# Performance work log

Hardware: AMD Instinct MI355X
Metric: run time of the kernel (lower is better)

Reference implementation:

```python
import math
import jax, jax.numpy as jnp
import numpy as np

IN_DIM, OUT_DIM = 256, 128
IN_SEQ, OUT_SEQ = 512, 512
NUM_BASIS = 16
LN_EPS = 1e-5
TWO_PI = 2.0 * math.pi


def _make_periods():
    # periods[i, j, g] = i*(out_dim*num_basis) + j*num_basis + g + 2
    i = np.arange(OUT_DIM)[:, None, None]
    j = np.arange(OUT_DIM)[None, :, None]
    g = np.arange(NUM_BASIS)[None, None, :]
    return jnp.asarray((i * (OUT_DIM * NUM_BASIS) + j * NUM_BASIS + g + 2).astype(np.float32))


def setup_inputs() -> dict:
    key = jax.random.key(0)
    kx, kM, kP, kL = jax.random.split(key, 4)
    x = jax.random.normal(kx, (IN_SEQ, IN_DIM), dtype=jnp.float32)
    M = jax.random.normal(kM, (OUT_DIM, IN_DIM), dtype=jnp.float32) * 0.5
    P = jax.random.normal(kP, (OUT_DIM, OUT_DIM, NUM_BASIS), dtype=jnp.float32) * 0.1
    Linker = jax.random.normal(kL, (IN_SEQ, OUT_SEQ), dtype=jnp.float32) * 0.1
    gamma = jnp.ones((OUT_DIM,), dtype=jnp.float32)
    beta = jnp.zeros((OUT_DIM,), dtype=jnp.float32)
    periods = _make_periods()  # (O, O, B) constant buffer
    return {"x": x, "M": M, "P": P, "Linker": Linker,
            "gamma": gamma, "beta": beta, "periods": periods}


def reference(x, M, P, Linker, gamma, beta, periods):
    # Projection: Z = x @ M.T  -> (S, O)
    Z = x @ M.T
    # LayerNorm over last dim
    mu = jnp.mean(Z, axis=-1, keepdims=True)
    var = jnp.mean(jnp.square(Z - mu), axis=-1, keepdims=True)
    Zn = (Z - mu) * jax.lax.rsqrt(var + LN_EPS) * gamma + beta
    # Position transform: T[k,i] = sum_{j,g} Zn[k,j] * P[i,j,g] * cos(2*pi*k / periods[i,j,g])
    k = jnp.arange(Z.shape[0], dtype=jnp.float32)[:, None, None, None]  # (S,1,1,1)
    phi = jnp.cos(TWO_PI * k / periods)  # (S, O, O, B)
    T = jnp.einsum('kj,ijg,kijg->ki', Zn, P, phi)  # (S, O)
    # Sequence transform: U = Linker.T @ T -> (out_seq, O)
    U = Linker.T @ T
    # 'shared' residual uses pre-LayerNorm projection x @ M.T
    residual = Linker.T @ Z
    return U + residual
```

## Files before the change

kernel.cpp:

```cpp
#include <hip/hip_runtime.h>

#define IN_DIM   256
#define OUT_DIM  128
#define IN_SEQ   512
#define OUT_SEQ  512
#define NUM_BASIS 16
#define LN_EPS   1e-5f

__global__ __launch_bounds__(256) void kA(const float* __restrict__ x,
                                          const float* __restrict__ M,
                                          const float* __restrict__ gamma,
                                          const float* __restrict__ beta,
                                          float* __restrict__ Zn,
                                          float* __restrict__ ZT) {
  const int k = blockIdx.x;
  const int t = threadIdx.x;
  __shared__ __align__(16) float xk[IN_DIM];
  __shared__ float red[256];
  __shared__ float stats[8];

  xk[t] = x[k * IN_DIM + t];
  __syncthreads();

  const int j = t & 127;
  const int h = t >> 7;
  const float4* __restrict__ M4 = reinterpret_cast<const float4*>(M + j * IN_DIM + h * 128);
  const float4* __restrict__ x4 = reinterpret_cast<const float4*>(xk + h * 128);
  float acc = 0.f;
#pragma unroll 8
  for (int c = 0; c < 32; ++c) {
    float4 m = M4[c];
    float4 xv = x4[c];
    acc = fmaf(m.x, xv.x, acc);
    acc = fmaf(m.y, xv.y, acc);
    acc = fmaf(m.z, xv.z, acc);
    acc = fmaf(m.w, xv.w, acc);
  }
  red[t] = acc;
  __syncthreads();

  float z = 0.f;
  if (t < 128) z = red[t] + red[t + 128];

  float s1 = (t < 128) ? z : 0.f;
  float s2 = (t < 128) ? z * z : 0.f;
#pragma unroll
  for (int m = 1; m < 64; m <<= 1) {
    s1 += __shfl_xor(s1, m);
    s2 += __shfl_xor(s2, m);
  }
  const int w = t >> 6;
  if ((t & 63) == 0) {
    stats[w] = s1;
    stats[4 + w] = s2;
  }
  __syncthreads();
  const float mu  = (stats[0] + stats[1] + stats[2] + stats[3]) * (1.f / 128.f);
  const float msq = (stats[4] + stats[5] + stats[6] + stats[7]) * (1.f / 128.f);
  const float rs  = rsqrtf(msq - mu * mu + LN_EPS);

  if (t < 128) {
    float zn = (z - mu) * rs * gamma[t] + beta[t];
    Zn[k * OUT_DIM + t] = zn;
    ZT[t * IN_SEQ + k] = z;
  }
}

__global__ __launch_bounds__(256) void kB(const float* __restrict__ P,
                                          const float* __restrict__ Zn,
                                          const float* __restrict__ ZT,
                                          float* __restrict__ V) {
  const int i  = blockIdx.y;
  const int k0 = blockIdx.x * 64;
  const int t  = threadIdx.x;

  __shared__ float2 pairs[OUT_DIM * NUM_BASIS];
  __shared__ float zn_lds[64 * 129];
  __shared__ float red[64 * 5];

  const float* __restrict__ Pi = P + i * (OUT_DIM * NUM_BASIS);
  const int pbase = i * (OUT_DIM * NUM_BASIS) + 2;
#pragma unroll
  for (int e = t; e < OUT_DIM * NUM_BASIS; e += 256) {
    float pw = Pi[e];
    float pinv = 1.0f / (float)(pbase + e);
    pairs[e] = make_float2(pw, pinv);
  }
#pragma unroll
  for (int m = 0; m < 32; ++m) {
    int idx = m * 256 + t;
    int r = idx >> 7;
    int j = idx & 127;
    zn_lds[r * 129 + j] = Zn[(k0 + r) * OUT_DIM + j];
  }
  __syncthreads();

  const int kl = t & 63;
  const int jq = t >> 6;
  const float kf = (float)(k0 + kl);
  const float* __restrict__ znrow = zn_lds + kl * 129;

  float acc = 0.f;
  for (int j = jq * 32; j < jq * 32 + 32; ++j) {
    float z = znrow[j];
    const float2* __restrict__ pp = pairs + j * NUM_BASIS;
    float accj = 0.f;
#pragma unroll
    for (int g = 0; g < NUM_BASIS; ++g) {
      float2 wv = pp[g];
      float ang = kf * wv.y;
      float fr  = __builtin_amdgcn_fractf(ang);
      float c   = __builtin_amdgcn_cosf(fr);
      accj = fmaf(wv.x, c, accj);
    }
    acc = fmaf(z, accj, acc);
  }

  red[kl * 5 + jq] = acc;
  __syncthreads();
  if (t < 64) {
    float s = red[t * 5 + 0] + red[t * 5 + 1] + red[t * 5 + 2] + red[t * 5 + 3];
    const int k = k0 + t;
    V[k * OUT_DIM + i] = s + ZT[i * IN_SEQ + k];
  }
}

__global__ __launch_bounds__(512) void kC(const float* __restrict__ L,
                                          const float* __restrict__ V,
                                          float* __restrict__ out) {
  const int s = blockIdx.x;
  const int t = threadIdx.x;
  const int i = t & 127;
  const int q = t >> 7;
  __shared__ float Lcol[IN_SEQ];
  __shared__ float red[4 * OUT_DIM];

  Lcol[t] = L[t * OUT_SEQ + s];
  __syncthreads();

  const int k0 = q * 128;
  float acc = 0.f;
#pragma unroll 8
  for (int kk = 0; kk < 128; ++kk) {
    const int k = k0 + kk;
    acc = fmaf(Lcol[k], V[k * OUT_DIM + i], acc);
  }
  red[q * OUT_DIM + i] = acc;
  __syncthreads();

  if (t < OUT_DIM) {
    out[s * OUT_DIM + t] =
        red[t] + red[OUT_DIM + t] + red[2 * OUT_DIM + t] + red[3 * OUT_DIM + t];
  }
}

extern "C" void kernel_launch(void* const* d_in, const int* in_sizes, int n_in,
                              void* d_out, int out_size, void* d_ws, size_t ws_size,
                              hipStream_t stream) {
  const float* x      = (const float*)d_in[0];
  const float* M      = (const float*)d_in[1];
  const float* P      = (const float*)d_in[2];
  const float* Linker = (const float*)d_in[3];
  const float* gamma  = (const float*)d_in[4];
  const float* beta   = (const float*)d_in[5];
  float* out = (float*)d_out;

  float* ws = (float*)d_ws;
  float* Zn = ws;
  float* ZT = ws + IN_SEQ * OUT_DIM;
  float* V  = ws + 2 * IN_SEQ * OUT_DIM;

  kA<<<dim3(IN_SEQ), dim3(256), 0, stream>>>(x, M, gamma, beta, Zn, ZT);
  kB<<<dim3(8, OUT_DIM), dim3(256), 0, stream>>>(P, Zn, ZT, V);
  kC<<<dim3(OUT_SEQ), dim3(512), 0, stream>>>(Linker, V, out);
}
```

Baseline: 43.96 us.

## Replace per-element cosine evaluation with a Chebyshev recurrence over sequence positions

The position-transform kernel is restructured so each thread owns one (i,j) pair and walks 64 consecutive k values. It uses the recurrence cos((k+1)θ) = 2cosθ·cos(kθ) − cos((k−1)θ) instead of a fract plus transcendental cos for every (k,j,g). Per-k partial sums are reduced across the j lanes with wave shuffles, and the shared-memory staging of P and Zn is removed. The aim is to drop the quarter-rate cosine cost. In exchange, the recurrence accumulates rounding error across steps, a reduction runs for every k, and the prefetch reads a few rows past the chunk end, including past the end of Zn for the last block.

```diff
diff --git a/kernel.cpp b/kernel.cpp
--- a/kernel.cpp
+++ b/kernel.cpp
@@ -6,6 +6,11 @@
 #define OUT_SEQ  512
 #define NUM_BASIS 16
 #define LN_EPS   1e-5f
+#define KC       64
+
+__device__ __forceinline__ float cosrev(float x) {
+  return __builtin_amdgcn_cosf(__builtin_amdgcn_fractf(x));
+}
 
 __global__ __launch_bounds__(256) void kA(const float* __restrict__ x,
                                           const float* __restrict__ M,
@@ -66,62 +71,76 @@
   }
 }
 
-__global__ __launch_bounds__(256) void kB(const float* __restrict__ P,
+__global__ __launch_bounds__(128) void kB(const float* __restrict__ P,
                                           const float* __restrict__ Zn,
                                           const float* __restrict__ ZT,
                                           float* __restrict__ V) {
   const int i  = blockIdx.y;
-  const int k0 = blockIdx.x * 64;
-  const int t  = threadIdx.x;
+  const int k0 = blockIdx.x * KC;
+  const int j  = threadIdx.x;
+  const int w  = j >> 6;
 
-  __shared__ float2 pairs[OUT_DIM * NUM_BASIS];
-  __shared__ float zn_lds[64 * 129];
-  __shared__ float red[64 * 5];
+  __shared__ float red[KC * 2];
 
-  const float* __restrict__ Pi = P + i * (OUT_DIM * NUM_BASIS);
-  const int pbase = i * (OUT_DIM * NUM_BASIS) + 2;
+  float Pv[NUM_BASIS], tc[NUM_BASIS], c0[NUM_BASIS], c1[NUM_BASIS];
+  {
+    const float4* __restrict__ P4 =
+        reinterpret_cast<const float4*>(P + (size_t)(i * OUT_DIM + j) * NUM_BASIS);
+    float4 pl[4] = {P4[0], P4[1], P4[2], P4[3]};
 #pragma unroll
-  for (int e = t; e < OUT_DIM * NUM_BASIS; e += 256) {
-    float pw = Pi[e];
-    float pinv = 1.0f / (float)(pbase + e);
-    pairs[e] = make_float2(pw, pinv);
+    for (int q = 0; q < 4; ++q) {
+      Pv[4 * q + 0] = pl[q].x;
+      Pv[4 * q + 1] = pl[q].y;
+      Pv[4 * q + 2] = pl[q].z;
+      Pv[4 * q + 3] = pl[q].w;
+    }
   }
+  const int pb = i * (OUT_DIM * NUM_BASIS) + j * NUM_BASIS + 2;
+  const float km1 = (float)(k0 - 1);
+  const float kcu = (float)k0;
 #pragma unroll
-  for (int m = 0; m < 32; ++m) {
-    int idx = m * 256 + t;
-    int r = idx >> 7;
-    int j = idx & 127;
-    zn_lds[r * 129 + j] = Zn[(k0 + r) * OUT_DIM + j];
-  }
-  __syncthreads();
-
-  const int kl = t & 63;
-  const int jq = t >> 6;
-  const float kf = (float)(k0 + kl);
-  const float* __restrict__ znrow = zn_lds + kl * 129;
-
-  float acc = 0.f;
-  for (int j = jq * 32; j < jq * 32 + 32; ++j) {
-    float z = znrow[j];
-    const float2* __restrict__ pp = pairs + j * NUM_BASIS;
-    float accj = 0.f;
-#pragma unroll
-    for (int g = 0; g < NUM_BASIS; ++g) {
-      float2 wv = pp[g];
-      float ang = kf * wv.y;
-      float fr  = __builtin_amdgcn_fractf(ang);
-      float c   = __builtin_amdgcn_cosf(fr);
-      accj = fmaf(wv.x, c, accj);
-    }
-    acc = fmaf(z, accj, acc);
+  for (int g = 0; g < NUM_BASIS; ++g) {
+    float pinv = 1.0f / (float)(pb + g);
+    tc[g] = 2.0f * __builtin_amdgcn_cosf(pinv);
+    c0[g] = cosrev(km1 * pinv);
+    c1[g] = cosrev(kcu * pinv);
   }
 
-  red[kl * 5 + jq] = acc;
+  const float* __restrict__ znj = Zn + j;
+  float buf[4];
+#pragma unroll
+  for (int r = 0; r < 4; ++r) buf[r] = znj[(k0 + r) * OUT_DIM];
+
+  for (int kg = 0; kg < KC / 4; ++kg) {
+    float nbuf[4];
+#pragma unroll
+    for (int r = 0; r < 4; ++r) {
+      nbuf[r] = znj[(k0 + (kg + 1) * 4 + r) * OUT_DIM];
+    }
+#pragma unroll
+    for (int r = 0; r < 4; ++r) {
+      float s = 0.f;
+#pragma unroll
+      for (int g = 0; g < NUM_BASIS; ++g) s = fmaf(Pv[g], c1[g], s);
+      float v = buf[r] * s;
+#pragma unroll
+      for (int m = 1; m < 64; m <<= 1) v += __shfl_xor(v, m);
+      if ((j & 63) == 0) red[(kg * 4 + r) * 2 + w] = v;
+#pragma unroll
+      for (int g = 0; g < NUM_BASIS; ++g) {
+        float cn = fmaf(tc[g], c1[g], -c0[g]);
+        c0[g] = c1[g];
+        c1[g] = cn;
+      }
+    }
+#pragma unroll
+    for (int r = 0; r < 4; ++r) buf[r] = nbuf[r];
+  }
+
   __syncthreads();
-  if (t < 64) {
-    float s = red[t * 5 + 0] + red[t * 5 + 1] + red[t * 5 + 2] + red[t * 5 + 3];
-    const int k = k0 + t;
-    V[k * OUT_DIM + i] = s + ZT[i * IN_SEQ + k];
+  if (j < KC) {
+    const int k = k0 + j;
+    V[k * OUT_DIM + i] = red[j * 2] + red[j * 2 + 1] + ZT[i * IN_SEQ + k];
   }
 }
 
@@ -171,6 +190,6 @@
   float* V  = ws + 2 * IN_SEQ * OUT_DIM;
 
   kA<<<dim3(IN_SEQ), dim3(256), 0, stream>>>(x, M, gamma, beta, Zn, ZT);
-  kB<<<dim3(8, OUT_DIM), dim3(256), 0, stream>>>(P, Zn, ZT, V);
+  kB<<<dim3(IN_SEQ / KC, OUT_DIM), dim3(128), 0, stream>>>(P, Zn, ZT, V);
   kC<<<dim3(OUT_SEQ), dim3(512), 0, stream>>>(Linker, V, out);
 }
```

Measured after the change: 43.32 us. No clear change (-1.5%).
